# Kernel tuning notes

Measured on AMD Instinct MI355X. Metric: run time of the kernel, lower is better.

## Reference

```python
import jax, jax.numpy as jnp
import numpy as np

TOP_K = 2  # num_experts_per_tok


def setup_inputs() -> dict:
    key = jax.random.key(0)
    ks = jax.random.split(key, 4)
    B, S, H, I, E = 4, 2048, 2048, 4096, 8
    std = 0.02
    hidden_states = jax.random.normal(ks[0], (B, S, H), dtype=jnp.float32)
    gate_w = jax.random.normal(ks[1], (E, H), dtype=jnp.float32) * std   # nn.Linear weight [E,H]
    wfc = jax.random.normal(ks[2], (E, I, H), dtype=jnp.float32) * std   # c_fc weight [E,out,in]
    bfc = jnp.zeros((E, I), dtype=jnp.float32)                           # bias zero-init
    wproj = jax.random.normal(ks[3], (E, H, I), dtype=jnp.float32) * std # c_proj weight
    bproj = jnp.zeros((E, H), dtype=jnp.float32)
    return {"hidden_states": hidden_states, "gate_w": gate_w, "wfc": wfc,
            "bfc": bfc, "wproj": wproj, "bproj": bproj}


def reference(hidden_states, gate_w, wfc, bfc, wproj, bproj):
    B, S, H = hidden_states.shape
    E = wfc.shape[0]
    x = hidden_states.reshape(-1, H)                      # [T, H]
    router_logits = x @ gate_w.T                          # [T, E]
    top_vals, top_idx = jax.lax.top_k(router_logits, TOP_K)
    router_weights = jax.nn.softmax(top_vals.astype(jnp.float32), axis=-1).astype(x.dtype)  # [T, k]
    out = jnp.zeros_like(x)
    # Loop over the small fixed set of experts; each token contributes with its
    # combined gate weight for that expert (0 if not routed there). Same math as
    # the torch gather/grouped-GEMM/scatter-add path.
    for e in range(E):
        gate_e = jnp.sum(jnp.where(top_idx == e, router_weights, 0.0), axis=-1)  # [T]
        h = jax.nn.gelu(x @ wfc[e].T + bfc[e], approximate=False)                # [T, I]
        y = h @ wproj[e].T + bproj[e]                                            # [T, H]
        out = out + gate_e[:, None] * y
    return out.reshape(B, S, H), router_logits
```

## Files before the change

### kernel.cpp

```cpp
#include <hip/hip_runtime.h>
#include <hip/hip_bf16.h>
#include <math.h>

#define NT 8192
#define HD 2048
#define ID 4096
#define NE 8
#define MAXSLOT 18432
#define MAXRB 72

typedef __bf16 bf16x8 __attribute__((ext_vector_type(8)));
typedef float f32x4 __attribute__((ext_vector_type(4)));

__device__ __forceinline__ float bf2f(unsigned short u){
  union{unsigned u; float f;} v; v.u = ((unsigned)u) << 16; return v.f;
}

__device__ __forceinline__ void gload_lds16(const void* g, void* l){
  __builtin_amdgcn_global_load_lds((const __attribute__((address_space(1))) void*)g,
                                   (__attribute__((address_space(3))) void*)l, 16, 0, 0);
}

__global__ __launch_bounds__(256) void cvt_kernel(const float* __restrict__ in,
                                                  __hip_bfloat16* __restrict__ outp, int n4){
  int i = blockIdx.x * blockDim.x + threadIdx.x;
  int stride = gridDim.x * blockDim.x;
  for (; i < n4; i += stride){
    float4 v = reinterpret_cast<const float4*>(in)[i];
    union{ushort4 u; __hip_bfloat16 h[4];} o;
    o.h[0] = __float2bfloat16(v.x); o.h[1] = __float2bfloat16(v.y);
    o.h[2] = __float2bfloat16(v.z); o.h[3] = __float2bfloat16(v.w);
    reinterpret_cast<ushort4*>(outp)[i] = o.u;
  }
}

__global__ __launch_bounds__(256) void gather_cvt_kernel(
    const float* __restrict__ x, const int* __restrict__ slotTok,
    __hip_bfloat16* __restrict__ xg)
{
  const int slot = blockIdx.x;
  const int c = threadIdx.x * 8;
  const int pr = slotTok[slot];
  ushort4* dst = reinterpret_cast<ushort4*>(xg + (long)slot * HD + c);
  if (pr < 0){
    ushort4 z = {0,0,0,0};
    dst[0] = z; dst[1] = z;
    return;
  }
  const float* src = x + (long)(pr >> 1) * HD + c;
  float4 v0 = reinterpret_cast<const float4*>(src)[0];
  float4 v1 = reinterpret_cast<const float4*>(src)[1];
  union{ushort4 u; __hip_bfloat16 h[4];} a, b;
  a.h[0]=__float2bfloat16(v0.x); a.h[1]=__float2bfloat16(v0.y);
  a.h[2]=__float2bfloat16(v0.z); a.h[3]=__float2bfloat16(v0.w);
  b.h[0]=__float2bfloat16(v1.x); b.h[1]=__float2bfloat16(v1.y);
  b.h[2]=__float2bfloat16(v1.z); b.h[3]=__float2bfloat16(v1.w);
  dst[0] = a.u; dst[1] = b.u;
}

__global__ __launch_bounds__(256) void router_kernel(
    const float* __restrict__ x, const float* __restrict__ gw,
    float* __restrict__ logits_out, int* __restrict__ tokExp,
    float* __restrict__ tokW, int* __restrict__ cnt)
{
  int wave = (blockIdx.x * blockDim.x + threadIdx.x) >> 6;
  int lane = threadIdx.x & 63;
  if (wave >= NT) return;
  const float* xr = x + (long)wave * HD;
  double acc[NE];
  #pragma unroll
  for (int e = 0; e < NE; e++) acc[e] = 0.0;
  for (int k = lane; k < HD; k += 64){
    double xv = (double)xr[k];
    #pragma unroll
    for (int e = 0; e < NE; e++) acc[e] += xv * (double)gw[e * HD + k];
  }
  #pragma unroll
  for (int e = 0; e < NE; e++){
    #pragma unroll
    for (int off = 32; off; off >>= 1) acc[e] += __shfl_down(acc[e], off, 64);
  }
  if (lane == 0){
    int e0 = 0; double v0 = acc[0];
    for (int e = 1; e < NE; e++) if (acc[e] > v0){ v0 = acc[e]; e0 = e; }
    int e1 = -1; double v1 = -1e300;
    for (int e = 0; e < NE; e++) if (e != e0 && acc[e] > v1){ v1 = acc[e]; e1 = e; }
    double ex = exp(v1 - v0);
    double s = 1.0 + ex;
    for (int e = 0; e < NE; e++) logits_out[wave * NE + e] = (float)acc[e];
    tokExp[wave * 2]     = e0; tokExp[wave * 2 + 1] = e1;
    tokW[wave * 2]       = (float)(1.0 / s);
    tokW[wave * 2 + 1]   = (float)(ex / s);
    atomicAdd(&cnt[e0], 1); atomicAdd(&cnt[e1], 1);
  }
}

__global__ void offsets_kernel(const int* __restrict__ cnt, int* __restrict__ padOff){
  if (threadIdx.x == 0 && blockIdx.x == 0){
    int o = 0;
    for (int e = 0; e < NE; e++){ padOff[e] = o; o += ((cnt[e] + 255) >> 8) << 8; }
    padOff[NE] = o;
  }
}

__global__ __launch_bounds__(256) void scatter_kernel(
    const int* __restrict__ tokExp, const int* __restrict__ padOff, int* cursor,
    int* __restrict__ slotTok)
{
  int t = blockIdx.x * blockDim.x + threadIdx.x;
  if (t >= NT) return;
  #pragma unroll
  for (int s = 0; s < 2; s++){
    int e = tokExp[t * 2 + s];
    int pos = atomicAdd(&cursor[e], 1);
    slotTok[padOff[e] + pos] = t * 2 + s;
  }
}


#define LDA(sb,m) (*reinterpret_cast<const bf16x8*>(&lds[(sb) + (wr*8+(m))*512 + laneF]))
#define LDB(sb,n) (*reinterpret_cast<const bf16x8*>(&lds[(sb) + 8192 + (wc*4+(n))*512 + laneF]))
#define STAGE(s,koff) do{ \
    __hip_bfloat16* dA_ = &lds[((s)&3)*16384 + w*1024]; \
    gload_lds16(aS0 + (koff), dA_); \
    gload_lds16(aS1 + (koff), dA_ + 512); \
    __hip_bfloat16* dB_ = dA_ + 8192; \
    gload_lds16(bS0 + (koff), dB_); \
    gload_lds16(bS1 + (koff), dB_ + 512); \
  }while(0)
#define MFMA16(M0,A0_,A1_,A2_,A3_) do{ \
    acc[(M0)+0][0] = __builtin_amdgcn_mfma_f32_16x16x32_bf16(A0_, bv0, acc[(M0)+0][0],0,0,0); \
    acc[(M0)+1][0] = __builtin_amdgcn_mfma_f32_16x16x32_bf16(A1_, bv0, acc[(M0)+1][0],0,0,0); \
    acc[(M0)+2][0] = __builtin_amdgcn_mfma_f32_16x16x32_bf16(A2_, bv0, acc[(M0)+2][0],0,0,0); \
    acc[(M0)+3][0] = __builtin_amdgcn_mfma_f32_16x16x32_bf16(A3_, bv0, acc[(M0)+3][0],0,0,0); \
    acc[(M0)+0][1] = __builtin_amdgcn_mfma_f32_16x16x32_bf16(A0_, bv1, acc[(M0)+0][1],0,0,0); \
    acc[(M0)+1][1] = __builtin_amdgcn_mfma_f32_16x16x32_bf16(A1_, bv1, acc[(M0)+1][1],0,0,0); \
    acc[(M0)+2][1] = __builtin_amdgcn_mfma_f32_16x16x32_bf16(A2_, bv1, acc[(M0)+2][1],0,0,0); \
    acc[(M0)+3][1] = __builtin_amdgcn_mfma_f32_16x16x32_bf16(A3_, bv1, acc[(M0)+3][1],0,0,0); \
    acc[(M0)+0][2] = __builtin_amdgcn_mfma_f32_16x16x32_bf16(A0_, bv2, acc[(M0)+0][2],0,0,0); \
    acc[(M0)+1][2] = __builtin_amdgcn_mfma_f32_16x16x32_bf16(A1_, bv2, acc[(M0)+1][2],0,0,0); \
    acc[(M0)+2][2] = __builtin_amdgcn_mfma_f32_16x16x32_bf16(A2_, bv2, acc[(M0)+2][2],0,0,0); \
    acc[(M0)+3][2] = __builtin_amdgcn_mfma_f32_16x16x32_bf16(A3_, bv2, acc[(M0)+3][2],0,0,0); \
    acc[(M0)+0][3] = __builtin_amdgcn_mfma_f32_16x16x32_bf16(A0_, bv3, acc[(M0)+0][3],0,0,0); \
    acc[(M0)+1][3] = __builtin_amdgcn_mfma_f32_16x16x32_bf16(A1_, bv3, acc[(M0)+1][3],0,0,0); \
    acc[(M0)+2][3] = __builtin_amdgcn_mfma_f32_16x16x32_bf16(A2_, bv3, acc[(M0)+2][3],0,0,0); \
    acc[(M0)+3][3] = __builtin_amdgcn_mfma_f32_16x16x32_bf16(A3_, bv3, acc[(M0)+3][3],0,0,0); \
  }while(0)

template<int AGATHER, int WSC, int EPI, int ND, int KD>
__global__ __launch_bounds__(512, 2) void moe_gemm12(
    const __hip_bfloat16* __restrict__ A,
    const __hip_bfloat16* __restrict__ W,
    const float* __restrict__ bias,
    const int* __restrict__ slotTok,
    const int* __restrict__ padOff,
    __hip_bfloat16* __restrict__ Yout)
{
  __shared__ __align__(16) __hip_bfloat16 lds[65536];
  const int bid = blockIdx.x;
  const int xcd = bid & 7;
  const int g   = bid >> 3;
  const int cb  = xcd + 8 * (g / MAXRB);
  const int rb  = g % MAXRB;
  if (rb * 256 >= padOff[NE]) return;
  int e = 0;
  #pragma unroll
  for (int i = 1; i < NE; i++) if (rb * 256 >= padOff[i]) e = i;

  const int tid  = threadIdx.x;
  const int lane = tid & 63;
  const int w    = tid >> 6;
  const int wr   = w >> 2;
  const int wc   = w & 3;

  const int r16s = lane >> 2;
  const int cgs  = (lane & 3) ^ ((r16s >> 1) & 3);
  const int r0 = rb * 256 + 32 * w + r16s;
  long ga0, ga1;
  if (AGATHER == 0){
    ga0 = r0; ga1 = r0 + 16;
  } else {
    int p0 = slotTok[r0], p1 = slotTok[r0 + 16];
    ga0 = p0 < 0 ? 0 : (AGATHER == 1 ? (p0 >> 1) : p0);
    ga1 = p1 < 0 ? 0 : (AGATHER == 1 ? (p1 >> 1) : p1);
  }
  const __hip_bfloat16* aS0 = A + ga0 * (long)KD + cgs * 8;
  const __hip_bfloat16* aS1 = A + ga1 * (long)KD + cgs * 8;
  const long rowB = (long)cb * 256 + 32 * w + r16s;
  const __hip_bfloat16* bS0 = W + (long)e * ND * KD + rowB * KD + cgs * 8;
  const __hip_bfloat16* bS1 = bS0 + 16 * (long)KD;

  const int r16f = lane & 15;
  const int chf  = lane >> 4;
  const int laneF = r16f * 32 + (chf ^ ((r16f >> 1) & 3)) * 8;

  f32x4 acc[8][4] = {};
  bf16x8 bv0, bv1, bv2, bv3;

  constexpr int NS = KD / 32;

  STAGE(0, 0);
  STAGE(1, 32);
  STAGE(2, 64);
  asm volatile("s_waitcnt vmcnt(8)" ::: "memory");
  __builtin_amdgcn_s_barrier();

  for (int t = 0; t < NS; ++t){
    const int sb = (t & 3) * 16384;
    {
      bf16x8 a0 = LDA(sb,0), a1 = LDA(sb,1), a2 = LDA(sb,2), a3 = LDA(sb,3);
      bv0 = LDB(sb,0); bv1 = LDB(sb,1); bv2 = LDB(sb,2); bv3 = LDB(sb,3);
      if (t + 3 < NS){ STAGE(t + 3, (long)(t + 3) * 32); }
      __builtin_amdgcn_s_barrier();
      asm volatile("s_waitcnt lgkmcnt(0)" ::: "memory");
      __builtin_amdgcn_s_setprio(1);
      MFMA16(0, a0, a1, a2, a3);
      __builtin_amdgcn_s_setprio(0);
      __builtin_amdgcn_s_barrier();
    }
    {
      bf16x8 a0 = LDA(sb,4), a1 = LDA(sb,5), a2 = LDA(sb,6), a3 = LDA(sb,7);
      __builtin_amdgcn_s_barrier();
      asm volatile("s_waitcnt lgkmcnt(0)" ::: "memory");
      __builtin_amdgcn_s_setprio(1);
      MFMA16(4, a0, a1, a2, a3);
      __builtin_amdgcn_s_setprio(0);
      const int rem = NS - 1 - t;
      if (rem >= 3)      asm volatile("s_waitcnt vmcnt(8)" ::: "memory");
      else if (rem == 2) asm volatile("s_waitcnt vmcnt(4)" ::: "memory");
      else if (rem == 1) asm volatile("s_waitcnt vmcnt(0)" ::: "memory");
      __builtin_amdgcn_s_barrier();
    }
  }

  const int colBase = cb * 256 + wc * 64 + (lane & 15);
  const int rowQ = (lane >> 4) * 4;
  float bb[4];
  #pragma unroll
  for (int n = 0; n < 4; n++) bb[n] = bias[(long)e * ND + colBase + n * 16];
  #pragma unroll
  for (int m = 0; m < 8; m++){
    const int grow = rb * 256 + wr * 128 + m * 16 + rowQ;
    #pragma unroll
    for (int r = 0; r < 4; r++){
      long orow;
      bool doW;
      if (WSC == 0){ orow = grow + r; doW = true; }
      else { int pr = slotTok[grow + r]; orow = pr; doW = (pr >= 0); }
      if (doW){
        #pragma unroll
        for (int n = 0; n < 4; n++){
          float v = acc[m][n][r] + bb[n];
          if (EPI == 0){
            v = 0.5f * v * (1.0f + erff(v * 0.70710678118654752f));
          }
          Yout[orow * ND + colBase + n * 16] = __float2bfloat16(v);
        }
      }
    }
  }
}

__global__ __launch_bounds__(256) void combine_kernel(
    const __hip_bfloat16* __restrict__ yb, const float* __restrict__ tokW,
    float* __restrict__ outp)
{
  const int t  = blockIdx.x;
  const int c0 = threadIdx.x * 8;
  const float w0 = tokW[t * 2], w1 = tokW[t * 2 + 1];
  const ushort4* p0 = reinterpret_cast<const ushort4*>(yb + (long)(2 * t) * HD + c0);
  const ushort4* p1 = reinterpret_cast<const ushort4*>(yb + (long)(2 * t + 1) * HD + c0);
  float4 o[2];
  #pragma unroll
  for (int h = 0; h < 2; h++){
    ushort4 a = p0[h], b = p1[h];
    o[h].x = w0 * bf2f(a.x) + w1 * bf2f(b.x);
    o[h].y = w0 * bf2f(a.y) + w1 * bf2f(b.y);
    o[h].z = w0 * bf2f(a.z) + w1 * bf2f(b.z);
    o[h].w = w0 * bf2f(a.w) + w1 * bf2f(b.w);
  }
  __syncthreads();
  float4* po = reinterpret_cast<float4*>(outp + (long)t * HD + c0);
  po[0] = o[0]; po[1] = o[1];
}

extern "C" void kernel_launch(void* const* d_in, const int* in_sizes, int n_in,
                              void* d_out, int out_size, void* d_ws, size_t ws_size,
                              hipStream_t stream)
{
  (void)in_sizes; (void)n_in; (void)out_size;
  const float* x     = (const float*)d_in[0];
  const float* gw    = (const float*)d_in[1];
  const float* wfc   = (const float*)d_in[2];
  const float* bfc   = (const float*)d_in[3];
  const float* wproj = (const float*)d_in[4];
  const float* bproj = (const float*)d_in[5];
  float* outp   = (float*)d_out;
  float* logits = outp + (size_t)NT * HD;
  __hip_bfloat16* yb = (__hip_bfloat16*)d_out;

  char* ws = (char*)d_ws;
  size_t off = 0;
  auto alloc = [&](size_t b){ void* p = ws + off; off += (b + 255) & ~(size_t)255; return p; };

  const size_t XG_B  = (size_t)MAXSLOT * HD * 2;
  const size_t HBS_B = (size_t)MAXSLOT * ID * 2;
  const size_t WB_B  = (size_t)NE * ID * HD * 2;
  const size_t MISC_B = (size_t)MAXSLOT*4 + NT*2*4 + NT*2*4 + 4096;
  const bool slotPath = (XG_B + HBS_B + WB_B + MISC_B + 4096) <= ws_size;

  __hip_bfloat16 *xg, *hb, *wB;
  if (slotPath){
    xg = (__hip_bfloat16*)alloc(XG_B);
    hb = (__hip_bfloat16*)alloc(HBS_B);
    wB = (__hip_bfloat16*)alloc(WB_B);
  } else {
    xg = (__hip_bfloat16*)alloc((size_t)NT * HD * 2);
    hb = (__hip_bfloat16*)alloc((size_t)NT * 2 * ID * 2);
    wB = (__hip_bfloat16*)alloc(WB_B);
  }
  int*   slotTok = (int*)alloc(MAXSLOT * 4);
  int*   tokExp  = (int*)alloc(NT * 2 * 4);
  float* tokW    = (float*)alloc(NT * 2 * 4);
  int*   meta    = (int*)alloc(256);
  int* cnt = meta; int* cursor = meta + 8; int* padOff = meta + 16;

  hipMemsetAsync(meta, 0, 256, stream);
  hipMemsetAsync(slotTok, 0xFF, MAXSLOT * 4, stream);

  router_kernel<<<NT / 4, 256, 0, stream>>>(x, gw, logits, tokExp, tokW, cnt);
  offsets_kernel<<<1, 64, 0, stream>>>(cnt, padOff);
  scatter_kernel<<<NT / 256, 256, 0, stream>>>(tokExp, padOff, cursor, slotTok);

  if (slotPath){
    gather_cvt_kernel<<<MAXSLOT, 256, 0, stream>>>(x, slotTok, xg);
    cvt_kernel<<<2048, 256, 0, stream>>>(wfc, wB, NE * ID * HD / 4);
    moe_gemm12<0, 0, 0, ID, HD><<<(ID / 256) * MAXRB, 512, 0, stream>>>(xg, wB, bfc, slotTok, padOff, hb);
    cvt_kernel<<<2048, 256, 0, stream>>>(wproj, wB, NE * HD * ID / 4);
    moe_gemm12<0, 1, 1, HD, ID><<<(HD / 256) * MAXRB, 512, 0, stream>>>(hb, wB, bproj, slotTok, padOff, yb);
  } else {
    cvt_kernel<<<2048, 256, 0, stream>>>(x, xg, NT * HD / 4);
    cvt_kernel<<<2048, 256, 0, stream>>>(wfc, wB, NE * ID * HD / 4);
    moe_gemm12<1, 1, 0, ID, HD><<<(ID / 256) * MAXRB, 512, 0, stream>>>(xg, wB, bfc, slotTok, padOff, hb);
    cvt_kernel<<<2048, 256, 0, stream>>>(wproj, wB, NE * HD * ID / 4);
    moe_gemm12<2, 1, 1, HD, ID><<<(HD / 256) * MAXRB, 512, 0, stream>>>(hb, wB, bproj, slotTok, padOff, yb);
  }

  combine_kernel<<<NT, 256, 0, stream>>>(yb, tokW, outp);
}
```

Measured before the change: 1.298 ms.

## Replace direct global-to-LDS loads with register-staged double-buffered pipeline

```diff
diff --git a/kernel.cpp b/kernel.cpp
--- a/kernel.cpp
+++ b/kernel.cpp
@@ -14,11 +14,6 @@
 
 __device__ __forceinline__ float bf2f(unsigned short u){
   union{unsigned u; float f;} v; v.u = ((unsigned)u) << 16; return v.f;
-}
-
-__device__ __forceinline__ void gload_lds16(const void* g, void* l){
-  __builtin_amdgcn_global_load_lds((const __attribute__((address_space(1))) void*)g,
-                                   (__attribute__((address_space(3))) void*)l, 16, 0, 0);
 }
 
 __global__ __launch_bounds__(256) void cvt_kernel(const float* __restrict__ in,
@@ -118,15 +113,20 @@
 }
 
 
-#define LDA(sb,m) (*reinterpret_cast<const bf16x8*>(&lds[(sb) + (wr*8+(m))*512 + laneF]))
-#define LDB(sb,n) (*reinterpret_cast<const bf16x8*>(&lds[(sb) + 8192 + (wc*4+(n))*512 + laneF]))
-#define STAGE(s,koff) do{ \
-    __hip_bfloat16* dA_ = &lds[((s)&3)*16384 + w*1024]; \
-    gload_lds16(aS0 + (koff), dA_); \
-    gload_lds16(aS1 + (koff), dA_ + 512); \
-    __hip_bfloat16* dB_ = dA_ + 8192; \
-    gload_lds16(bS0 + (koff), dB_); \
-    gload_lds16(bS1 + (koff), dB_ + 512); \
+#define LDA(bufb,m) (*reinterpret_cast<const bf16x8*>(&lds[(bufb)*16384 + (wr*8+(m))*512 + laneF]))
+#define LDB(bufb,n) (*reinterpret_cast<const bf16x8*>(&lds[(bufb)*16384 + 8192 + (wc*4+(n))*512 + laneF]))
+#define LOADR(A0r,A1r,B0r,B1r,koff) do{ \
+    A0r = *reinterpret_cast<const float4*>(aU0 + (koff)); \
+    A1r = *reinterpret_cast<const float4*>(aU1 + (koff)); \
+    B0r = *reinterpret_cast<const float4*>(bU0 + (koff)); \
+    B1r = *reinterpret_cast<const float4*>(bU1 + (koff)); \
+  }while(0)
+#define WRITE(bufb,A0r,A1r,B0r,B1r) do{ \
+    __hip_bfloat16* dA_ = &lds[(bufb)*16384 + w*1024 + wrElem]; \
+    *reinterpret_cast<float4*>(dA_)       = A0r; \
+    *reinterpret_cast<float4*>(dA_ + 512) = A1r; \
+    *reinterpret_cast<float4*>(dA_ + 8192)       = B0r; \
+    *reinterpret_cast<float4*>(dA_ + 8192 + 512) = B1r; \
   }while(0)
 #define MFMA16(M0,A0_,A1_,A2_,A3_) do{ \
     acc[(M0)+0][0] = __builtin_amdgcn_mfma_f32_16x16x32_bf16(A0_, bv0, acc[(M0)+0][0],0,0,0); \
@@ -148,7 +148,7 @@
   }while(0)
 
 template<int AGATHER, int WSC, int EPI, int ND, int KD>
-__global__ __launch_bounds__(512, 2) void moe_gemm12(
+__global__ __launch_bounds__(512, 2) void moe_gemmR(
     const __hip_bfloat16* __restrict__ A,
     const __hip_bfloat16* __restrict__ W,
     const float* __restrict__ bias,
@@ -156,7 +156,7 @@
     const int* __restrict__ padOff,
     __hip_bfloat16* __restrict__ Yout)
 {
-  __shared__ __align__(16) __hip_bfloat16 lds[65536];
+  __shared__ __align__(16) __hip_bfloat16 lds[32768];
   const int bid = blockIdx.x;
   const int xcd = bid & 7;
   const int g   = bid >> 3;
@@ -174,7 +174,7 @@
   const int wc   = w & 3;
 
   const int r16s = lane >> 2;
-  const int cgs  = (lane & 3) ^ ((r16s >> 1) & 3);
+  const int cch  = lane & 3;
   const int r0 = rb * 256 + 32 * w + r16s;
   long ga0, ga1;
   if (AGATHER == 0){
@@ -184,51 +184,65 @@
     ga0 = p0 < 0 ? 0 : (AGATHER == 1 ? (p0 >> 1) : p0);
     ga1 = p1 < 0 ? 0 : (AGATHER == 1 ? (p1 >> 1) : p1);
   }
-  const __hip_bfloat16* aS0 = A + ga0 * (long)KD + cgs * 8;
-  const __hip_bfloat16* aS1 = A + ga1 * (long)KD + cgs * 8;
+  const __hip_bfloat16* aU0 = A + ga0 * (long)KD + cch * 8;
+  const __hip_bfloat16* aU1 = A + ga1 * (long)KD + cch * 8;
   const long rowB = (long)cb * 256 + 32 * w + r16s;
-  const __hip_bfloat16* bS0 = W + (long)e * ND * KD + rowB * KD + cgs * 8;
-  const __hip_bfloat16* bS1 = bS0 + 16 * (long)KD;
-
+  const __hip_bfloat16* bU0 = W + (long)e * ND * KD + rowB * KD + cch * 8;
+  const __hip_bfloat16* bU1 = bU0 + 16 * (long)KD;
+
+  const int wrElem = r16s * 32 + (cch ^ ((r16s >> 1) & 3)) * 8;
   const int r16f = lane & 15;
-  const int chf  = lane >> 4;
-  const int laneF = r16f * 32 + (chf ^ ((r16f >> 1) & 3)) * 8;
+  const int laneF = r16f * 32 + (((lane >> 4) ^ ((r16f >> 1) & 3))) * 8;
 
   f32x4 acc[8][4] = {};
   bf16x8 bv0, bv1, bv2, bv3;
 
   constexpr int NS = KD / 32;
 
-  STAGE(0, 0);
-  STAGE(1, 32);
-  STAGE(2, 64);
-  asm volatile("s_waitcnt vmcnt(8)" ::: "memory");
+  float4 pa0, pa1, pb0, pb1, qa0, qa1, qb0, qb1;
+  LOADR(pa0, pa1, pb0, pb1, 0);
+  LOADR(qa0, qa1, qb0, qb1, 32);
+  WRITE(0, pa0, pa1, pb0, pb1);
+  asm volatile("s_waitcnt lgkmcnt(0)" ::: "memory");
   __builtin_amdgcn_s_barrier();
 
-  for (int t = 0; t < NS; ++t){
-    const int sb = (t & 3) * 16384;
+  for (int t = 0; t < NS; t += 2){
     {
-      bf16x8 a0 = LDA(sb,0), a1 = LDA(sb,1), a2 = LDA(sb,2), a3 = LDA(sb,3);
-      bv0 = LDB(sb,0); bv1 = LDB(sb,1); bv2 = LDB(sb,2); bv3 = LDB(sb,3);
-      if (t + 3 < NS){ STAGE(t + 3, (long)(t + 3) * 32); }
+      bf16x8 a0 = LDA(0,0), a1 = LDA(0,1), a2 = LDA(0,2), a3 = LDA(0,3);
+      bv0 = LDB(0,0); bv1 = LDB(0,1); bv2 = LDB(0,2); bv3 = LDB(0,3);
+      if (t + 2 < NS){ LOADR(pa0, pa1, pb0, pb1, (long)(t + 2) * 32); }
       __builtin_amdgcn_s_barrier();
       asm volatile("s_waitcnt lgkmcnt(0)" ::: "memory");
       __builtin_amdgcn_s_setprio(1);
       MFMA16(0, a0, a1, a2, a3);
       __builtin_amdgcn_s_setprio(0);
       __builtin_amdgcn_s_barrier();
+      bf16x8 c0 = LDA(0,4), c1 = LDA(0,5), c2 = LDA(0,6), c3 = LDA(0,7);
+      WRITE(1, qa0, qa1, qb0, qb1);
+      asm volatile("s_waitcnt lgkmcnt(0)" ::: "memory");
+      __builtin_amdgcn_s_barrier();
+      __builtin_amdgcn_s_setprio(1);
+      MFMA16(4, c0, c1, c2, c3);
+      __builtin_amdgcn_s_setprio(0);
+      __builtin_amdgcn_s_barrier();
     }
     {
-      bf16x8 a0 = LDA(sb,4), a1 = LDA(sb,5), a2 = LDA(sb,6), a3 = LDA(sb,7);
+      bf16x8 a0 = LDA(1,0), a1 = LDA(1,1), a2 = LDA(1,2), a3 = LDA(1,3);
+      bv0 = LDB(1,0); bv1 = LDB(1,1); bv2 = LDB(1,2); bv3 = LDB(1,3);
+      if (t + 3 < NS){ LOADR(qa0, qa1, qb0, qb1, (long)(t + 3) * 32); }
       __builtin_amdgcn_s_barrier();
       asm volatile("s_waitcnt lgkmcnt(0)" ::: "memory");
       __builtin_amdgcn_s_setprio(1);
-      MFMA16(4, a0, a1, a2, a3);
+      MFMA16(0, a0, a1, a2, a3);
       __builtin_amdgcn_s_setprio(0);
-      const int rem = NS - 1 - t;
-      if (rem >= 3)      asm volatile("s_waitcnt vmcnt(8)" ::: "memory");
-      else if (rem == 2) asm volatile("s_waitcnt vmcnt(4)" ::: "memory");
-      else if (rem == 1) asm volatile("s_waitcnt vmcnt(0)" ::: "memory");
+      __builtin_amdgcn_s_barrier();
+      bf16x8 c0 = LDA(1,4), c1 = LDA(1,5), c2 = LDA(1,6), c3 = LDA(1,7);
+      if (t + 2 < NS){ WRITE(0, pa0, pa1, pb0, pb1); }
+      asm volatile("s_waitcnt lgkmcnt(0)" ::: "memory");
+      __builtin_amdgcn_s_barrier();
+      __builtin_amdgcn_s_setprio(1);
+      MFMA16(4, c0, c1, c2, c3);
+      __builtin_amdgcn_s_setprio(0);
       __builtin_amdgcn_s_barrier();
     }
   }
@@ -335,15 +349,15 @@
   if (slotPath){
     gather_cvt_kernel<<<MAXSLOT, 256, 0, stream>>>(x, slotTok, xg);
     cvt_kernel<<<2048, 256, 0, stream>>>(wfc, wB, NE * ID * HD / 4);
-    moe_gemm12<0, 0, 0, ID, HD><<<(ID / 256) * MAXRB, 512, 0, stream>>>(xg, wB, bfc, slotTok, padOff, hb);
+    moe_gemmR<0, 0, 0, ID, HD><<<(ID / 256) * MAXRB, 512, 0, stream>>>(xg, wB, bfc, slotTok, padOff, hb);
     cvt_kernel<<<2048, 256, 0, stream>>>(wproj, wB, NE * HD * ID / 4);
-    moe_gemm12<0, 1, 1, HD, ID><<<(HD / 256) * MAXRB, 512, 0, stream>>>(hb, wB, bproj, slotTok, padOff, yb);
+    moe_gemmR<0, 1, 1, HD, ID><<<(HD / 256) * MAXRB, 512, 0, stream>>>(hb, wB, bproj, slotTok, padOff, yb);
   } else {
     cvt_kernel<<<2048, 256, 0, stream>>>(x, xg, NT * HD / 4);
     cvt_kernel<<<2048, 256, 0, stream>>>(wfc, wB, NE * ID * HD / 4);
-    moe_gemm12<1, 1, 0, ID, HD><<<(ID / 256) * MAXRB, 512, 0, stream>>>(xg, wB, bfc, slotTok, padOff, hb);
+    moe_gemmR<1, 1, 0, ID, HD><<<(ID / 256) * MAXRB, 512, 0, stream>>>(xg, wB, bfc, slotTok, padOff, hb);
     cvt_kernel<<<2048, 256, 0, stream>>>(wproj, wB, NE * HD * ID / 4);
-    moe_gemm12<2, 1, 1, HD, ID><<<(HD / 256) * MAXRB, 512, 0, stream>>>(hb, wB, bproj, slotTok, padOff, yb);
+    moe_gemmR<2, 1, 1, HD, ID><<<(HD / 256) * MAXRB, 512, 0, stream>>>(hb, wB, bproj, slotTok, padOff, yb);
   }
 
   combine_kernel<<<NT, 256, 0, stream>>>(yb, tokW, outp);
```

After: 1.514 ms. +16.6%, slower.
